# Performance work log

Hardware: AMD Instinct MI355X
Metric: run time of the kernel (lower is better)

The kernel has to match this reference:

```python
import jax, jax.numpy as jnp
import numpy as np

EMBED_DIM = 128
NUM_HEADS = 4
HEAD_DIM = EMBED_DIM // NUM_HEADS
B, S = 2, 1024


def setup_inputs() -> dict:
    key = jax.random.key(0)
    ks = jax.random.split(key, 9)
    sc = 1.0 / np.sqrt(EMBED_DIM)
    x = jax.random.normal(ks[0], (B, S, EMBED_DIM), dtype=jnp.float32)
    # torch nn.Linear weights: (out_features, in_features)
    Wq = jax.random.uniform(ks[1], (EMBED_DIM, EMBED_DIM), jnp.float32, -sc, sc)
    bq = jax.random.uniform(ks[2], (EMBED_DIM,), jnp.float32, -sc, sc)
    Wk = jax.random.uniform(ks[3], (EMBED_DIM, EMBED_DIM), jnp.float32, -sc, sc)
    bk = jax.random.uniform(ks[4], (EMBED_DIM,), jnp.float32, -sc, sc)
    Wv = jax.random.uniform(ks[5], (EMBED_DIM, EMBED_DIM), jnp.float32, -sc, sc)
    bv = jax.random.uniform(ks[6], (EMBED_DIM,), jnp.float32, -sc, sc)
    Wo = jax.random.uniform(ks[7], (EMBED_DIM, EMBED_DIM), jnp.float32, -sc, sc)
    bo = jax.random.uniform(ks[8], (EMBED_DIM,), jnp.float32, -sc, sc)
    return {"x": x, "Wq": Wq, "bq": bq, "Wk": Wk, "bk": bk,
            "Wv": Wv, "bv": bv, "Wo": Wo, "bo": bo}


def _heads(y):
    # (B,S,E) -> (B,H,S,D)
    return y.reshape(B, S, NUM_HEADS, HEAD_DIM).transpose(0, 2, 1, 3)


def reference(x, Wq, bq, Wk, bk, Wv, bv, Wo, bo):
    q = _heads(x @ Wq.T + bq)  # (B,H,S,D)
    k = _heads(x @ Wk.T + bk)
    v = _heads(x @ Wv.T + bv)
    # ultrametric (Chebyshev / max-abs) distance: (B,H,S,S)
    dist = jnp.max(jnp.abs(q[:, :, :, None, :] - k[:, :, None, :, :]), axis=-1)
    attn = jax.nn.softmax(-dist, axis=-1)
    attended = jnp.einsum('bhst,bhtd->bhsd', attn, v)
    attended = attended.transpose(0, 2, 1, 3).reshape(B, S, EMBED_DIM)
    return attended @ Wo.T + bo
```

## Files before the change

kernel.cpp:

```cpp
#include <hip/hip_runtime.h>
#include <hip/hip_bf16.h>

#define B_ 2
#define S_ 1024
#define E_ 128
#define H_ 4
#define D_ 32
#define BHSD (B_ * H_ * S_ * D_)
#define LOG2E 1.44269504088896f

__global__ __launch_bounds__(128) void qkv_kernel(
    const float* __restrict__ x,
    const float* __restrict__ Wq, const float* __restrict__ bq,
    const float* __restrict__ Wk, const float* __restrict__ bk,
    const float* __restrict__ Wv, const float* __restrict__ bv,
    float* __restrict__ ws) {
  const int mat = blockIdx.y;
  const float* W    = (mat == 0) ? Wq : (mat == 1) ? Wk : Wv;
  const float* bias = (mat == 0) ? bq : (mat == 1) ? bk : bv;
  const float scale = (mat == 2) ? 1.0f : LOG2E;
  float* outbase = ws + (size_t)mat * BHSD;

  const int row0 = blockIdx.x * 8;
  const int t = threadIdx.x;

  __shared__ __align__(16) float xs[8 * E_];
  const float4* xg = (const float4*)(x + (size_t)row0 * E_);
  float4* xs4 = (float4*)xs;
  #pragma unroll
  for (int i = 0; i < 2; ++i) xs4[t + i * 128] = xg[t + i * 128];
  __syncthreads();

  const int col = t;
  const float4* W4 = (const float4*)(W + (size_t)col * E_);

  float acc[8];
  #pragma unroll
  for (int r = 0; r < 8; ++r) acc[r] = 0.f;

  #pragma unroll 4
  for (int c4 = 0; c4 < E_ / 4; ++c4) {
    float4 w = W4[c4];
    #pragma unroll
    for (int r = 0; r < 8; ++r) {
      float4 xv = xs4[r * (E_ / 4) + c4];
      acc[r] += xv.x * w.x + xv.y * w.y + xv.z * w.z + xv.w * w.w;
    }
  }

  const float bcol = bias[col];
  const int h = col >> 5, d = col & 31;
  #pragma unroll
  for (int r = 0; r < 8; ++r) {
    int row = row0 + r;
    int b = row >> 10, s = row & 1023;
    outbase[(((size_t)(b * H_ + h)) * S_ + s) * D_ + d] = (acc[r] + bcol) * scale;
  }
}

#define SMEM_BYTES (8 * 32 * 36 * 4 + 8 * 32 * 4)

__global__ __launch_bounds__(512)
__attribute__((amdgpu_waves_per_eu(4, 4)))
void attn_kernel(
    const float* __restrict__ qg, const float* __restrict__ kg,
    const float* __restrict__ vg,
    float* __restrict__ part_o, float* __restrict__ part_l) {
  __shared__ __align__(16) char smem[SMEM_BYTES];
  float* ks = (float*)smem;
  float (*sm_o)[32][36] = (float (*)[32][36])smem;
  float* sm_l = (float*)(smem + 8 * 32 * 36 * 4);

  const int rt = blockIdx.x >> 2;
  const int kc = blockIdx.x & 3;
  const int t = threadIdx.x;
  const int w = t >> 6;
  const int lane = t & 63;
  const int h = lane >> 5;
  const int r = lane & 31;
  const int bh = rt >> 5;
  const int srow = (rt & 31) * 32 + r;

  const float* kbase = kg + (size_t)bh * S_ * D_;
  const float* vbase = vg + (size_t)bh * S_ * D_;

  {
    const float4* kgt = (const float4*)(kbase + (size_t)kc * 256 * D_);
    float4* ks4 = (float4*)ks;
    #pragma unroll
    for (int i = 0; i < 4; ++i) {
      int f = t + i * 512;
      ks4[f] = kgt[f];
    }
  }

  const float* qrow = qg + ((size_t)bh * S_ + srow) * D_ + h * 16;
  float4 q0 = *(const float4*)(qrow + 0);
  float4 q1 = *(const float4*)(qrow + 4);
  float4 q2 = *(const float4*)(qrow + 8);
  float4 q3 = *(const float4*)(qrow + 12);

  float o[16];
  #pragma unroll
  for (int i = 0; i < 16; ++i) o[i] = 0.f;
  float l = 0.f;

  __syncthreads();

  const float* kLds = ks + (size_t)(w * 32) * D_ + h * 16;
  const float* vGlb = vbase + ((size_t)(kc * 256) + w * 32) * D_ + h * 16;

  float4 ka0 = *(const float4*)(kLds + 0);
  float4 ka1 = *(const float4*)(kLds + 4);
  float4 ka2 = *(const float4*)(kLds + 8);
  float4 ka3 = *(const float4*)(kLds + 12);
  float4 va0 = *(const float4*)(vGlb + 0);
  float4 va1 = *(const float4*)(vGlb + 4);
  float4 va2 = *(const float4*)(vGlb + 8);
  float4 va3 = *(const float4*)(vGlb + 12);

  #pragma unroll 4
  for (int jj = 0; jj < 32; ++jj) {
    const float* kn = kLds + (size_t)(jj + 1) * D_;
    const float* vn = vGlb + (size_t)(jj + 1) * D_;
    float4 kb0 = *(const float4*)(kn + 0);
    float4 kb1 = *(const float4*)(kn + 4);
    float4 kb2 = *(const float4*)(kn + 8);
    float4 kb3 = *(const float4*)(kn + 12);
    float4 vb0 = *(const float4*)(vn + 0);
    float4 vb1 = *(const float4*)(vn + 4);
    float4 vb2 = *(const float4*)(vn + 8);
    float4 vb3 = *(const float4*)(vn + 12);

    float c0 = 0.f, c1 = 0.f;
    c0 = fmaxf(c0, fmaxf(fabsf(q0.x - ka0.x), fabsf(q0.y - ka0.y)));
    c1 = fmaxf(c1, fmaxf(fabsf(q0.z - ka0.z), fabsf(q0.w - ka0.w)));
    c0 = fmaxf(c0, fmaxf(fabsf(q1.x - ka1.x), fabsf(q1.y - ka1.y)));
    c1 = fmaxf(c1, fmaxf(fabsf(q1.z - ka1.z), fabsf(q1.w - ka1.w)));
    c0 = fmaxf(c0, fmaxf(fabsf(q2.x - ka2.x), fabsf(q2.y - ka2.y)));
    c1 = fmaxf(c1, fmaxf(fabsf(q2.z - ka2.z), fabsf(q2.w - ka2.w)));
    c0 = fmaxf(c0, fmaxf(fabsf(q3.x - ka3.x), fabsf(q3.y - ka3.y)));
    c1 = fmaxf(c1, fmaxf(fabsf(q3.z - ka3.z), fabsf(q3.w - ka3.w)));
    float dh = fmaxf(c0, c1);
    float dist = fmaxf(dh, __shfl_xor(dh, 32));
    float p = exp2f(-dist);
    l += p;

    o[ 0] = fmaf(p, va0.x, o[ 0]); o[ 1] = fmaf(p, va0.y, o[ 1]);
    o[ 2] = fmaf(p, va0.z, o[ 2]); o[ 3] = fmaf(p, va0.w, o[ 3]);
    o[ 4] = fmaf(p, va1.x, o[ 4]); o[ 5] = fmaf(p, va1.y, o[ 5]);
    o[ 6] = fmaf(p, va1.z, o[ 6]); o[ 7] = fmaf(p, va1.w, o[ 7]);
    o[ 8] = fmaf(p, va2.x, o[ 8]); o[ 9] = fmaf(p, va2.y, o[ 9]);
    o[10] = fmaf(p, va2.z, o[10]); o[11] = fmaf(p, va2.w, o[11]);
    o[12] = fmaf(p, va3.x, o[12]); o[13] = fmaf(p, va3.y, o[13]);
    o[14] = fmaf(p, va3.z, o[14]); o[15] = fmaf(p, va3.w, o[15]);

    ka0 = kb0; ka1 = kb1; ka2 = kb2; ka3 = kb3;
    va0 = vb0; va1 = vb1; va2 = vb2; va3 = vb3;
  }

  __syncthreads();

  {
    float* dst = &sm_o[w][r][h * 16];
    #pragma unroll
    for (int e = 0; e < 4; ++e)
      *(float4*)(dst + e * 4) = make_float4(o[e*4+0], o[e*4+1], o[e*4+2], o[e*4+3]);
    if (h == 0) sm_l[w * 32 + r] = l;
  }
  __syncthreads();

  #pragma unroll
  for (int pi = 0; pi < 2; ++pi) {
    const int id = t + pi * 512;
    const int rr = id >> 5, dd = id & 31;
    float s = 0.f;
    #pragma unroll
    for (int ww = 0; ww < 8; ++ww) s += sm_o[ww][rr][dd];
    part_o[((size_t)(rt * 4 + kc) * 32 + rr) * 32 + dd] = s;
  }
  if (t < 32) {
    float s = 0.f;
    #pragma unroll
    for (int ww = 0; ww < 8; ++ww) s += sm_l[ww * 32 + t];
    part_l[(size_t)(rt * 4 + kc) * 32 + t] = s;
  }
}

__global__ __launch_bounds__(128) void out_kernel(
    const float* __restrict__ part_o, const float* __restrict__ part_l,
    const float* __restrict__ Wo, const float* __restrict__ bo,
    float* __restrict__ out) {
  const int row0 = blockIdx.x * 8;
  const int t = threadIdx.x;

  __shared__ __align__(16) float xs[8 * E_];

  const int e = t;
  const int h = e >> 5, d = e & 31;
  #pragma unroll
  for (int i = 0; i < 8; ++i) {
    const int r = row0 + i;
    const int b = r >> 10, s = r & 1023;
    const int rt = (b * H_ + h) * 32 + (s >> 5);
    const int lrow = s & 31;
    float acc = 0.f, lsum = 0.f;
    #pragma unroll
    for (int kc = 0; kc < 4; ++kc) {
      const size_t base = (size_t)(rt * 4 + kc) * 32 + lrow;
      acc  += part_o[base * 32 + d];
      lsum += part_l[base];
    }
    xs[i * E_ + e] = acc / lsum;
  }
  __syncthreads();

  const int col = t;
  const float4* W4 = (const float4*)(Wo + (size_t)col * E_);
  const float4* xs4 = (const float4*)xs;

  float acc[8];
  #pragma unroll
  for (int r = 0; r < 8; ++r) acc[r] = 0.f;

  #pragma unroll 4
  for (int c4 = 0; c4 < E_ / 4; ++c4) {
    float4 w = W4[c4];
    #pragma unroll
    for (int r = 0; r < 8; ++r) {
      float4 xv = xs4[r * (E_ / 4) + c4];
      acc[r] += xv.x * w.x + xv.y * w.y + xv.z * w.z + xv.w * w.w;
    }
  }

  const float bcol = bo[col];
  #pragma unroll
  for (int r = 0; r < 8; ++r)
    out[(size_t)(row0 + r) * E_ + col] = acc[r] + bcol;
}

extern "C" void kernel_launch(void* const* d_in, const int* in_sizes, int n_in,
                              void* d_out, int out_size, void* d_ws, size_t ws_size,
                              hipStream_t stream) {
  const float* x  = (const float*)d_in[0];
  const float* Wq = (const float*)d_in[1];
  const float* bq = (const float*)d_in[2];
  const float* Wk = (const float*)d_in[3];
  const float* bk = (const float*)d_in[4];
  const float* Wv = (const float*)d_in[5];
  const float* bv = (const float*)d_in[6];
  const float* Wo = (const float*)d_in[7];
  const float* bo = (const float*)d_in[8];
  float* ws  = (float*)d_ws;
  float* out = (float*)d_out;

  float* qd = ws;
  float* kd = ws + (size_t)BHSD;
  float* vd = ws + 2 * (size_t)BHSD;
  float* part_o = ws + 3 * (size_t)BHSD;
  float* part_l = part_o + (size_t)256 * 4 * 32 * 32;

  qkv_kernel<<<dim3((B_ * S_) / 8, 3), 128, 0, stream>>>(x, Wq, bq, Wk, bk, Wv, bv, ws);
  attn_kernel<<<dim3(256 * 4), 512, 0, stream>>>(qd, kd, vd, part_o, part_l);
  out_kernel<<<dim3((B_ * S_) / 8), 128, 0, stream>>>(part_o, part_l, Wo, bo, out);
}
```

Before: 63.00 us.

## Batch attention inner loop in groups of 8 keys and double rows per projection block

The attention inner loop now handles keys in groups of eight: it computes eight Chebyshev distances, then eight exponentials, then eight V accumulations, replacing the one-ahead register prefetch. This gives more independent loads and ALU work to overlap shuffle, exp and memory latency. The fixed waves-per-EU attribute is removed so the compiler can use more registers. The QKV and output projection kernels each process 16 rows per block instead of 8, halving the grid and reusing each weight load across more rows, at some cost in occupancy and parallelism.

```diff
diff --git a/kernel.cpp b/kernel.cpp
--- a/kernel.cpp
+++ b/kernel.cpp
@@ -21,28 +21,28 @@
   const float scale = (mat == 2) ? 1.0f : LOG2E;
   float* outbase = ws + (size_t)mat * BHSD;
 
-  const int row0 = blockIdx.x * 8;
+  const int row0 = blockIdx.x * 16;
   const int t = threadIdx.x;
 
-  __shared__ __align__(16) float xs[8 * E_];
+  __shared__ __align__(16) float xs[16 * E_];
   const float4* xg = (const float4*)(x + (size_t)row0 * E_);
   float4* xs4 = (float4*)xs;
   #pragma unroll
-  for (int i = 0; i < 2; ++i) xs4[t + i * 128] = xg[t + i * 128];
+  for (int i = 0; i < 4; ++i) xs4[t + i * 128] = xg[t + i * 128];
   __syncthreads();
 
   const int col = t;
   const float4* W4 = (const float4*)(W + (size_t)col * E_);
 
-  float acc[8];
-  #pragma unroll
-  for (int r = 0; r < 8; ++r) acc[r] = 0.f;
-
-  #pragma unroll 4
+  float acc[16];
+  #pragma unroll
+  for (int r = 0; r < 16; ++r) acc[r] = 0.f;
+
+  #pragma unroll 2
   for (int c4 = 0; c4 < E_ / 4; ++c4) {
     float4 w = W4[c4];
     #pragma unroll
-    for (int r = 0; r < 8; ++r) {
+    for (int r = 0; r < 16; ++r) {
       float4 xv = xs4[r * (E_ / 4) + c4];
       acc[r] += xv.x * w.x + xv.y * w.y + xv.z * w.z + xv.w * w.w;
     }
@@ -51,7 +51,7 @@
   const float bcol = bias[col];
   const int h = col >> 5, d = col & 31;
   #pragma unroll
-  for (int r = 0; r < 8; ++r) {
+  for (int r = 0; r < 16; ++r) {
     int row = row0 + r;
     int b = row >> 10, s = row & 1023;
     outbase[(((size_t)(b * H_ + h)) * S_ + s) * D_ + d] = (acc[r] + bcol) * scale;
@@ -61,7 +61,6 @@
 #define SMEM_BYTES (8 * 32 * 36 * 4 + 8 * 32 * 4)
 
 __global__ __launch_bounds__(512)
-__attribute__((amdgpu_waves_per_eu(4, 4)))
 void attn_kernel(
     const float* __restrict__ qg, const float* __restrict__ kg,
     const float* __restrict__ vg,
@@ -110,53 +109,53 @@
   const float* kLds = ks + (size_t)(w * 32) * D_ + h * 16;
   const float* vGlb = vbase + ((size_t)(kc * 256) + w * 32) * D_ + h * 16;
 
-  float4 ka0 = *(const float4*)(kLds + 0);
-  float4 ka1 = *(const float4*)(kLds + 4);
-  float4 ka2 = *(const float4*)(kLds + 8);
-  float4 ka3 = *(const float4*)(kLds + 12);
-  float4 va0 = *(const float4*)(vGlb + 0);
-  float4 va1 = *(const float4*)(vGlb + 4);
-  float4 va2 = *(const float4*)(vGlb + 8);
-  float4 va3 = *(const float4*)(vGlb + 12);
-
-  #pragma unroll 4
-  for (int jj = 0; jj < 32; ++jj) {
-    const float* kn = kLds + (size_t)(jj + 1) * D_;
-    const float* vn = vGlb + (size_t)(jj + 1) * D_;
-    float4 kb0 = *(const float4*)(kn + 0);
-    float4 kb1 = *(const float4*)(kn + 4);
-    float4 kb2 = *(const float4*)(kn + 8);
-    float4 kb3 = *(const float4*)(kn + 12);
-    float4 vb0 = *(const float4*)(vn + 0);
-    float4 vb1 = *(const float4*)(vn + 4);
-    float4 vb2 = *(const float4*)(vn + 8);
-    float4 vb3 = *(const float4*)(vn + 12);
-
-    float c0 = 0.f, c1 = 0.f;
-    c0 = fmaxf(c0, fmaxf(fabsf(q0.x - ka0.x), fabsf(q0.y - ka0.y)));
-    c1 = fmaxf(c1, fmaxf(fabsf(q0.z - ka0.z), fabsf(q0.w - ka0.w)));
-    c0 = fmaxf(c0, fmaxf(fabsf(q1.x - ka1.x), fabsf(q1.y - ka1.y)));
-    c1 = fmaxf(c1, fmaxf(fabsf(q1.z - ka1.z), fabsf(q1.w - ka1.w)));
-    c0 = fmaxf(c0, fmaxf(fabsf(q2.x - ka2.x), fabsf(q2.y - ka2.y)));
-    c1 = fmaxf(c1, fmaxf(fabsf(q2.z - ka2.z), fabsf(q2.w - ka2.w)));
-    c0 = fmaxf(c0, fmaxf(fabsf(q3.x - ka3.x), fabsf(q3.y - ka3.y)));
-    c1 = fmaxf(c1, fmaxf(fabsf(q3.z - ka3.z), fabsf(q3.w - ka3.w)));
-    float dh = fmaxf(c0, c1);
-    float dist = fmaxf(dh, __shfl_xor(dh, 32));
-    float p = exp2f(-dist);
-    l += p;
-
-    o[ 0] = fmaf(p, va0.x, o[ 0]); o[ 1] = fmaf(p, va0.y, o[ 1]);
-    o[ 2] = fmaf(p, va0.z, o[ 2]); o[ 3] = fmaf(p, va0.w, o[ 3]);
-    o[ 4] = fmaf(p, va1.x, o[ 4]); o[ 5] = fmaf(p, va1.y, o[ 5]);
-    o[ 6] = fmaf(p, va1.z, o[ 6]); o[ 7] = fmaf(p, va1.w, o[ 7]);
-    o[ 8] = fmaf(p, va2.x, o[ 8]); o[ 9] = fmaf(p, va2.y, o[ 9]);
-    o[10] = fmaf(p, va2.z, o[10]); o[11] = fmaf(p, va2.w, o[11]);
-    o[12] = fmaf(p, va3.x, o[12]); o[13] = fmaf(p, va3.y, o[13]);
-    o[14] = fmaf(p, va3.z, o[14]); o[15] = fmaf(p, va3.w, o[15]);
-
-    ka0 = kb0; ka1 = kb1; ka2 = kb2; ka3 = kb3;
-    va0 = vb0; va1 = vb1; va2 = vb2; va3 = vb3;
+  for (int b = 0; b < 4; ++b) {
+    const int b8 = b * 8;
+
+    float dh[8];
+    #pragma unroll
+    for (int i = 0; i < 8; ++i) {
+      const float* kr = kLds + (size_t)(b8 + i) * D_;
+      float4 k0 = *(const float4*)(kr + 0);
+      float4 k1 = *(const float4*)(kr + 4);
+      float4 k2 = *(const float4*)(kr + 8);
+      float4 k3 = *(const float4*)(kr + 12);
+      float c0 = fmaxf(fabsf(q0.x - k0.x), fabsf(q0.y - k0.y));
+      float c1 = fmaxf(fabsf(q0.z - k0.z), fabsf(q0.w - k0.w));
+      c0 = fmaxf(c0, fmaxf(fabsf(q1.x - k1.x), fabsf(q1.y - k1.y)));
+      c1 = fmaxf(c1, fmaxf(fabsf(q1.z - k1.z), fabsf(q1.w - k1.w)));
+      c0 = fmaxf(c0, fmaxf(fabsf(q2.x - k2.x), fabsf(q2.y - k2.y)));
+      c1 = fmaxf(c1, fmaxf(fabsf(q2.z - k2.z), fabsf(q2.w - k2.w)));
+      c0 = fmaxf(c0, fmaxf(fabsf(q3.x - k3.x), fabsf(q3.y - k3.y)));
+      c1 = fmaxf(c1, fmaxf(fabsf(q3.z - k3.z), fabsf(q3.w - k3.w)));
+      dh[i] = fmaxf(c0, c1);
+    }
+
+    float p[8];
+    #pragma unroll
+    for (int i = 0; i < 8; ++i) {
+      float d2 = fmaxf(dh[i], __shfl_xor(dh[i], 32));
+      p[i] = exp2f(-d2);
+    }
+
+    #pragma unroll
+    for (int i = 0; i < 8; ++i) {
+      const float* vr = vGlb + (size_t)(b8 + i) * D_;
+      float4 v0 = *(const float4*)(vr + 0);
+      float4 v1 = *(const float4*)(vr + 4);
+      float4 v2 = *(const float4*)(vr + 8);
+      float4 v3 = *(const float4*)(vr + 12);
+      const float pi = p[i];
+      l += pi;
+      o[ 0] = fmaf(pi, v0.x, o[ 0]); o[ 1] = fmaf(pi, v0.y, o[ 1]);
+      o[ 2] = fmaf(pi, v0.z, o[ 2]); o[ 3] = fmaf(pi, v0.w, o[ 3]);
+      o[ 4] = fmaf(pi, v1.x, o[ 4]); o[ 5] = fmaf(pi, v1.y, o[ 5]);
+      o[ 6] = fmaf(pi, v1.z, o[ 6]); o[ 7] = fmaf(pi, v1.w, o[ 7]);
+      o[ 8] = fmaf(pi, v2.x, o[ 8]); o[ 9] = fmaf(pi, v2.y, o[ 9]);
+      o[10] = fmaf(pi, v2.z, o[10]); o[11] = fmaf(pi, v2.w, o[11]);
+      o[12] = fmaf(pi, v3.x, o[12]); o[13] = fmaf(pi, v3.y, o[13]);
+      o[14] = fmaf(pi, v3.z, o[14]); o[15] = fmaf(pi, v3.w, o[15]);
+    }
   }
 
   __syncthreads();
@@ -191,15 +190,15 @@
     const float* __restrict__ part_o, const float* __restrict__ part_l,
     const float* __restrict__ Wo, const float* __restrict__ bo,
     float* __restrict__ out) {
-  const int row0 = blockIdx.x * 8;
+  const int row0 = blockIdx.x * 16;
   const int t = threadIdx.x;
 
-  __shared__ __align__(16) float xs[8 * E_];
+  __shared__ __align__(16) float xs[16 * E_];
 
   const int e = t;
   const int h = e >> 5, d = e & 31;
   #pragma unroll
-  for (int i = 0; i < 8; ++i) {
+  for (int i = 0; i < 16; ++i) {
     const int r = row0 + i;
     const int b = r >> 10, s = r & 1023;
     const int rt = (b * H_ + h) * 32 + (s >> 5);
@@ -219,15 +218,15 @@
   const float4* W4 = (const float4*)(Wo + (size_t)col * E_);
   const float4* xs4 = (const float4*)xs;
 
-  float acc[8];
-  #pragma unroll
-  for (int r = 0; r < 8; ++r) acc[r] = 0.f;
-
-  #pragma unroll 4
+  float acc[16];
+  #pragma unroll
+  for (int r = 0; r < 16; ++r) acc[r] = 0.f;
+
+  #pragma unroll 2
   for (int c4 = 0; c4 < E_ / 4; ++c4) {
     float4 w = W4[c4];
     #pragma unroll
-    for (int r = 0; r < 8; ++r) {
+    for (int r = 0; r < 16; ++r) {
       float4 xv = xs4[r * (E_ / 4) + c4];
       acc[r] += xv.x * w.x + xv.y * w.y + xv.z * w.z + xv.w * w.w;
     }
@@ -235,7 +234,7 @@
 
   const float bcol = bo[col];
   #pragma unroll
-  for (int r = 0; r < 8; ++r)
+  for (int r = 0; r < 16; ++r)
     out[(size_t)(row0 + r) * E_ + col] = acc[r] + bcol;
 }
 
@@ -260,7 +259,7 @@
   float* part_o = ws + 3 * (size_t)BHSD;
   float* part_l = part_o + (size_t)256 * 4 * 32 * 32;
 
-  qkv_kernel<<<dim3((B_ * S_) / 8, 3), 128, 0, stream>>>(x, Wq, bq, Wk, bk, Wv, bv, ws);
+  qkv_kernel<<<dim3((B_ * S_) / 16, 3), 128, 0, stream>>>(x, Wq, bq, Wk, bk, Wv, bv, ws);
   attn_kernel<<<dim3(256 * 4), 512, 0, stream>>>(qd, kd, vd, part_o, part_l);
-  out_kernel<<<dim3((B_ * S_) / 8), 128, 0, stream>>>(part_o, part_l, Wo, bo, out);
-}
+  out_kernel<<<dim3((B_ * S_) / 16), 128, 0, stream>>>(part_o, part_l, Wo, bo, out);
+}
```

Result: slower. 91.34 us (+45.0%).
